# Kernel optimization log

Measured on AMD Instinct MI355X. Metric: run time of the kernel, lower is better.

The kernel has to match this reference:

```python
import jax, jax.numpy as jnp
import numpy as np

B, KD, VD = 65536, 512, 512

def setup_inputs() -> dict:
    key = jax.random.key(0)
    ks = jax.random.split(key, 5)
    return {
        "k": jax.random.normal(ks[0], (B, KD), jnp.float32),
        "v": jax.random.normal(ks[1], (B, VD), jnp.float32),
        "W": jax.random.normal(ks[2], (VD, KD), jnp.float32) * 0.02,  # memory.weight
        "S": jax.random.normal(ks[3], (VD, KD), jnp.float32) * 0.01,  # momentum buffer
        "gate_w": jax.random.normal(ks[4], (3, KD), jnp.float32) * 0.02,
        "gate_b": jnp.full((3,), 0.5, jnp.float32),  # nn.init.constant_(bias, 0.5)
    }

def reference(k, v, W, S, gate_w, gate_b):
    sg = jax.lax.stop_gradient
    # memory lookup: Linear(key_dim -> val_dim), no bias
    retrieved = k @ W.T                           # (B, VD)
    diff = retrieved - sg(v)
    loss_memory = jnp.mean(diff * diff)
    # --- TTT update (training path; all detached from autodiff in torch) ---
    # autograd.grad of mse(memory(k), v) w.r.t. W is analytically an outer product:
    # grad = 2/(B*VD) * (k @ W.T - v).T @ k
    d = sg(diff)                                  # loss_ttt uses detached k, v -> same residual values
    grad = (2.0 / (B * VD)) * (d.T @ sg(k))       # (VD, KD)
    # gates from batch-mean key
    gates = jax.nn.sigmoid(gate_w @ sg(jnp.mean(k, axis=0)) + gate_b)  # (3,)
    alpha, eta, theta = gates[0], gates[1], gates[2]
    new_S = eta * sg(S) - theta * grad            # momentum decay + gradient step
    new_W = (1.0 - alpha) * sg(W) + new_S         # gated weight decay + momentum write
    return retrieved, loss_memory, new_W, new_S
```

## Files before the change

kernel.cpp:

```cpp
#include <hip/hip_runtime.h>
#include <hip/hip_bf16.h>

typedef __attribute__((ext_vector_type(8))) short bf16x8;
typedef __attribute__((ext_vector_type(4))) float f32x4;
typedef unsigned int u32;
typedef unsigned short u16;

#define NB 65536
#define NKD 512
#define NVD 512

#define WS_COLSUM 262144
#define WS_LOSS   262656
#define WS_DIFFT_BYTES 1056768

#define OUT_LOSS 33554432
#define OUT_W    33554433
#define OUT_S    33816577

__device__ inline u32 pkbf2(float a, float b) {
    __hip_bfloat162 h2 = __float22bfloat162_rn(make_float2(a, b));
    u32 r;
    __builtin_memcpy(&r, &h2, 4);
    return r;
}

__device__ inline void async16(const u16* g, u16* l) {
    __builtin_amdgcn_global_load_lds(
        (const __attribute__((address_space(1))) u32*)g,
        (__attribute__((address_space(3))) u32*)l, 16, 0, 0);
}

#define PA 72
#define PT 136

__global__ __launch_bounds__(256, 3)
void k1_gemm1(const float* __restrict__ kmat, const float* __restrict__ vmat,
              const float* __restrict__ Wmat, float* __restrict__ out,
              float* __restrict__ ws, u16* __restrict__ diffT) {
    __shared__ u16 sm[18432];
    __shared__ float lred[4];

    const int tid = threadIdx.x;
    const int bx = blockIdx.x;
    const int xcd = bx & 7, slot = bx >> 3;
    const int rowtile = xcd * 64 + (slot >> 2), ntile = slot & 3;
    const long b0 = (long)rowtile * 128;
    const int vd0 = ntile * 128;
    const int wv = tid >> 6, lane = tid & 63;
    const int wm = wv & 1, wn = wv >> 1;
    const int col = lane & 15, kg = lane >> 4;

    const int srow = tid >> 4;
    const int scol = (tid & 15) * 4;

    f32x4 acc[4][4] = {};

    const float* gA = kmat + (b0 + srow) * 512 + scol;
    const float* gB = Wmat + (long)(vd0 + srow) * 512 + scol;

    float4 ra[8], rb[8];
#pragma unroll
    for (int i = 0; i < 8; ++i) {
        ra[i] = *(const float4*)(gA + (long)i * 16 * 512);
        rb[i] = *(const float4*)(gB + (long)i * 16 * 512);
    }

    for (int it = 0; it < 8; ++it) {
        __syncthreads();
#pragma unroll
        for (int i = 0; i < 8; ++i) {
            int r = i * 16 + srow;
            *(uint2*)&sm[r * PA + scol] = make_uint2(pkbf2(ra[i].x, ra[i].y), pkbf2(ra[i].z, ra[i].w));
            *(uint2*)&sm[9216 + r * PA + scol] = make_uint2(pkbf2(rb[i].x, rb[i].y), pkbf2(rb[i].z, rb[i].w));
        }
        __syncthreads();
        if (it < 7) {
            gA += 64; gB += 64;
#pragma unroll
            for (int i = 0; i < 8; ++i) {
                ra[i] = *(const float4*)(gA + (long)i * 16 * 512);
                rb[i] = *(const float4*)(gB + (long)i * 16 * 512);
            }
        }
#pragma unroll
        for (int kk = 0; kk < 2; ++kk) {
            bf16x8 af[4], bfr[4];
#pragma unroll
            for (int i = 0; i < 4; ++i)
                af[i] = *(const bf16x8*)&sm[(wm * 64 + i * 16 + col) * PA + kk * 32 + kg * 8];
#pragma unroll
            for (int j = 0; j < 4; ++j)
                bfr[j] = *(const bf16x8*)&sm[9216 + (wn * 64 + j * 16 + col) * PA + kk * 32 + kg * 8];
#pragma unroll
            for (int i = 0; i < 4; ++i)
#pragma unroll
                for (int j = 0; j < 4; ++j)
                    acc[i][j] = __builtin_amdgcn_mfma_f32_16x16x32_bf16(af[i], bfr[j], acc[i][j], 0, 0, 0);
        }
    }

    __syncthreads();
    u16* smT = sm;

    float lossp = 0.f;
    const int rg = lane >> 4;
#pragma unroll
    for (int i = 0; i < 4; ++i) {
#pragma unroll
        for (int j = 0; j < 4; ++j) {
            int r0 = wm * 64 + i * 16 + rg * 4;
            int c  = wn * 64 + j * 16 + col;
            long gb = b0 + r0;
            float dd[4];
#pragma unroll
            for (int r = 0; r < 4; ++r) {
                float rv = acc[i][j][r];
                long gidx = (gb + r) * 512 + vd0 + c;
                out[gidx] = rv;
                float dv = rv - vmat[gidx];
                lossp += dv * dv;
                dd[r] = dv;
            }
            *(u32*)&smT[c * PT + r0]     = pkbf2(dd[0], dd[1]);
            *(u32*)&smT[c * PT + r0 + 2] = pkbf2(dd[2], dd[3]);
        }
    }

#pragma unroll
    for (int m = 32; m; m >>= 1) lossp += __shfl_xor(lossp, m);
    if (lane == 0) lred[wv] = lossp;
    __syncthreads();
    if (tid == 0) atomicAdd(&ws[WS_LOSS], lred[0] + lred[1] + lred[2] + lred[3]);

    {
        const int c = tid >> 1, h = tid & 1;
        const u16* src = &smT[c * PT + h * 64];
        u16* dst = diffT + ((long)(vd0 + c) << 16) + b0 + h * 64;
#pragma unroll
        for (int q = 0; q < 8; ++q) {
            uint4 t4 = *(const uint4*)(src + q * 8);
            *(uint4*)(dst + q * 8) = t4;
        }
    }
}

__global__ __launch_bounds__(256, 3)
void k2_grad(const u16* __restrict__ diffT, const float* __restrict__ kmat,
             float* __restrict__ ws) {
    __shared__ u16 sm[25600];

    const int tid = threadIdx.x;
    const int bx = blockIdx.x;
    const int xcd = bx & 7, slot = bx >> 3;
    const int chunk = xcd * 4 + (slot >> 4), tile = slot & 15;
    const int vd0 = (tile >> 2) * 128, kd0 = (tile & 3) * 128;
    const long b0 = (long)chunk * 2048;
    const int wv = tid >> 6, lane = tid & 63;
    const int wm = wv & 1, wn = wv >> 1;
    const int col = lane & 15, kg = lane >> 4;

    const int bcol = (tid & 63) * 2;
    const int bq = wv * 16;

    f32x4 acc[4][4] = {};
    float cs0 = 0.f, cs1 = 0.f;

    const int rowb0 = wv * 32;
    const u16* gAit = diffT + ((long)(vd0 + rowb0 + (lane >> 3)) << 16) + b0 + (lane & 7) * 8;
    const float* gk0 = kmat + (b0 + bq) * 512 + kd0 + bcol;

    float2 rB[16];
#pragma unroll
    for (int q = 0; q < 4; ++q)
        async16(gAit + ((long)(q * 8) << 16), &sm[(rowb0 + q * 8) * 64]);
#pragma unroll
    for (int i = 0; i < 16; ++i) rB[i] = *(const float2*)(gk0 + (long)i * 512);

    for (int it = 0; it < 32; ++it) {
        u16* As = sm + (it & 1) * 8192;
        u16* Bs = sm + 16384;
        __syncthreads();
        {
#pragma unroll
            for (int i = 0; i < 16; ++i) { cs0 += rB[i].x; cs1 += rB[i].y; }
            u32 p0[8], p1[8];
#pragma unroll
            for (int i = 0; i < 8; ++i) {
                p0[i] = pkbf2(rB[2 * i].x, rB[2 * i + 1].x);
                p1[i] = pkbf2(rB[2 * i].y, rB[2 * i + 1].y);
            }
            *(uint4*)&Bs[bcol * PA + bq]           = make_uint4(p0[0], p0[1], p0[2], p0[3]);
            *(uint4*)&Bs[bcol * PA + bq + 8]       = make_uint4(p0[4], p0[5], p0[6], p0[7]);
            *(uint4*)&Bs[(bcol + 1) * PA + bq]     = make_uint4(p1[0], p1[1], p1[2], p1[3]);
            *(uint4*)&Bs[(bcol + 1) * PA + bq + 8] = make_uint4(p1[4], p1[5], p1[6], p1[7]);
        }
        __syncthreads();
        if (it < 31) {
            u16* An = sm + ((it + 1) & 1) * 8192;
            const u16* gan = gAit + (it + 1) * 64;
#pragma unroll
            for (int q = 0; q < 4; ++q)
                async16(gan + ((long)(q * 8) << 16), &An[(rowb0 + q * 8) * 64]);
            const float* gkn = gk0 + (long)(it + 1) * 64 * 512;
#pragma unroll
            for (int i = 0; i < 16; ++i) rB[i] = *(const float2*)(gkn + (long)i * 512);
        }
#pragma unroll
        for (int kk = 0; kk < 2; ++kk) {
            bf16x8 af[4], bfr[4];
#pragma unroll
            for (int i = 0; i < 4; ++i)
                af[i] = *(const bf16x8*)&As[(wm * 64 + i * 16 + col) * 64 + kk * 32 + kg * 8];
#pragma unroll
            for (int j = 0; j < 4; ++j)
                bfr[j] = *(const bf16x8*)&Bs[(wn * 64 + j * 16 + col) * PA + kk * 32 + kg * 8];
#pragma unroll
            for (int i = 0; i < 4; ++i)
#pragma unroll
                for (int j = 0; j < 4; ++j)
                    acc[i][j] = __builtin_amdgcn_mfma_f32_16x16x32_bf16(af[i], bfr[j], acc[i][j], 0, 0, 0);
        }
    }

    const int rg = lane >> 4;
#pragma unroll
    for (int i = 0; i < 4; ++i)
#pragma unroll
        for (int j = 0; j < 4; ++j)
#pragma unroll
            for (int r = 0; r < 4; ++r) {
                int vd = vd0 + wm * 64 + i * 16 + rg * 4 + r;
                int kd = kd0 + wn * 64 + j * 16 + col;
                atomicAdd(&ws[vd * 512 + kd], acc[i][j][r]);
            }

    if (vd0 == 0) {
        __syncthreads();
        float* cred = (float*)sm;
        cred[bcol * 4 + wv] = cs0;
        cred[(bcol + 1) * 4 + wv] = cs1;
        __syncthreads();
        if (tid < 128) {
            float s = cred[tid * 4] + cred[tid * 4 + 1] + cred[tid * 4 + 2] + cred[tid * 4 + 3];
            atomicAdd(&ws[WS_COLSUM + kd0 + tid], s);
        }
    }
}

__global__ __launch_bounds__(256)
void k3_final(const float* __restrict__ Wmat, const float* __restrict__ Smat,
              const float* __restrict__ gw, const float* __restrict__ gb,
              const float* __restrict__ ws, float* __restrict__ out) {
    __shared__ float gates[3];
    const int tid = threadIdx.x;
    if (tid < 64) {
        float d0 = 0.f, d1 = 0.f, d2 = 0.f;
#pragma unroll
        for (int i = 0; i < 8; ++i) {
            int kd = i * 64 + tid;
            float km = ws[WS_COLSUM + kd] * (1.0f / 65536.0f);
            d0 += gw[kd] * km;
            d1 += gw[512 + kd] * km;
            d2 += gw[1024 + kd] * km;
        }
#pragma unroll
        for (int m = 32; m; m >>= 1) {
            d0 += __shfl_xor(d0, m);
            d1 += __shfl_xor(d1, m);
            d2 += __shfl_xor(d2, m);
        }
        if (tid == 0) {
            gates[0] = 1.f / (1.f + __expf(-(d0 + gb[0])));
            gates[1] = 1.f / (1.f + __expf(-(d1 + gb[1])));
            gates[2] = 1.f / (1.f + __expf(-(d2 + gb[2])));
        }
    }
    __syncthreads();
    const float alpha = gates[0], eta = gates[1], theta = gates[2];
    const int i = blockIdx.x * 256 + tid;
    float g = ws[i] * 5.9604644775390625e-8f;
    float ns = eta * Smat[i] - theta * g;
    out[OUT_S + i] = ns;
    out[OUT_W + i] = (1.f - alpha) * Wmat[i] + ns;
    if (blockIdx.x == 0 && tid == 0)
        out[OUT_LOSS] = ws[WS_LOSS] * 2.98023223876953125e-8f;
}

extern "C" void kernel_launch(void* const* d_in, const int* in_sizes, int n_in,
                              void* d_out, int out_size, void* d_ws, size_t ws_size,
                              hipStream_t stream) {
    const float* k  = (const float*)d_in[0];
    const float* v  = (const float*)d_in[1];
    const float* W  = (const float*)d_in[2];
    const float* S  = (const float*)d_in[3];
    const float* gw = (const float*)d_in[4];
    const float* gb = (const float*)d_in[5];
    float* out = (float*)d_out;
    float* ws  = (float*)d_ws;
    u16* diffT = (u16*)((char*)d_ws + WS_DIFFT_BYTES);

    hipMemsetAsync(d_ws, 0, (WS_LOSS + 1) * sizeof(float), stream);

    hipLaunchKernelGGL(k1_gemm1, dim3(2048), dim3(256), 0, stream, k, v, W, out, ws, diffT);
    hipLaunchKernelGGL(k2_grad,  dim3(512),  dim3(256), 0, stream, diffT, k, ws);
    hipLaunchKernelGGL(k3_final, dim3(1024), dim3(256), 0, stream, W, S, gw, gb, ws, out);
}
```

Before: 490.6 us.

## Compute gradient via k^T k and v^T k Gram matrices, fusing both GEMM passes

Rewrites the gradient algebraically as W·(kᵀk) − vᵀk. Both Gram matrices are computed straight from the inputs in the same launch as the retrieval GEMM, so the bf16 transposed diff buffer and its round trip through memory are gone. The final kernel now does a 512x512x512 matmul (W times kᵀk) on CUDA cores before the elementwise update. In exchange the reduction work doubles, since two Gram matrices replace one diffᵀk, and the final kernel becomes compute heavy. Accuracy also changes because the residual is no longer formed explicitly before bf16 rounding.

```diff
diff --git a/kernel.cpp b/kernel.cpp
--- a/kernel.cpp
+++ b/kernel.cpp
@@ -6,17 +6,17 @@
 typedef unsigned int u32;
 typedef unsigned short u16;
 
-#define NB 65536
-#define NKD 512
-#define NVD 512
-
+#define WS_G2     0
 #define WS_COLSUM 262144
 #define WS_LOSS   262656
-#define WS_DIFFT_BYTES 1056768
+#define WS_G1     262912
+#define WS_END    525056
 
 #define OUT_LOSS 33554432
 #define OUT_W    33554433
 #define OUT_S    33816577
+
+#define PA 72
 
 __device__ inline u32 pkbf2(float a, float b) {
     __hip_bfloat162 h2 = __float22bfloat162_rn(make_float2(a, b));
@@ -25,225 +25,200 @@
     return r;
 }
 
-__device__ inline void async16(const u16* g, u16* l) {
-    __builtin_amdgcn_global_load_lds(
-        (const __attribute__((address_space(1))) u32*)g,
-        (__attribute__((address_space(3))) u32*)l, 16, 0, 0);
-}
-
-#define PA 72
-#define PT 136
-
 __global__ __launch_bounds__(256, 3)
-void k1_gemm1(const float* __restrict__ kmat, const float* __restrict__ vmat,
-              const float* __restrict__ Wmat, float* __restrict__ out,
-              float* __restrict__ ws, u16* __restrict__ diffT) {
+void k12(const float* __restrict__ kmat, const float* __restrict__ vmat,
+         const float* __restrict__ Wmat, float* __restrict__ out,
+         float* __restrict__ ws) {
     __shared__ u16 sm[18432];
-    __shared__ float lred[4];
+    __shared__ float red[4];
 
     const int tid = threadIdx.x;
     const int bx = blockIdx.x;
-    const int xcd = bx & 7, slot = bx >> 3;
-    const int rowtile = xcd * 64 + (slot >> 2), ntile = slot & 3;
-    const long b0 = (long)rowtile * 128;
-    const int vd0 = ntile * 128;
+    const int g24 = bx / 24;
+    const int u   = bx - g24 * 24;
     const int wv = tid >> 6, lane = tid & 63;
     const int wm = wv & 1, wn = wv >> 1;
     const int col = lane & 15, kg = lane >> 4;
-
-    const int srow = tid >> 4;
-    const int scol = (tid & 15) * 4;
-
-    f32x4 acc[4][4] = {};
-
-    const float* gA = kmat + (b0 + srow) * 512 + scol;
-    const float* gB = Wmat + (long)(vd0 + srow) * 512 + scol;
-
-    float4 ra[8], rb[8];
-#pragma unroll
-    for (int i = 0; i < 8; ++i) {
-        ra[i] = *(const float4*)(gA + (long)i * 16 * 512);
-        rb[i] = *(const float4*)(gB + (long)i * 16 * 512);
-    }
-
-    for (int it = 0; it < 8; ++it) {
+    const int rg = lane >> 4;
+
+    if (u < 16) {
+        const int idx = g24 * 16 + u;
+        const int xcd = idx & 7, slot = idx >> 3;
+        const int rowtile = xcd * 64 + (slot >> 2), ntile = slot & 3;
+        const long b0 = (long)rowtile * 128;
+        const int vd0 = ntile * 128;
+
+        const int srow = tid >> 4;
+        const int scol = (tid & 15) * 4;
+
+        f32x4 acc[4][4] = {};
+
+        const float* gA = kmat + (b0 + srow) * 512 + scol;
+        const float* gB = Wmat + (long)(vd0 + srow) * 512 + scol;
+
+        float4 ra[8], rb[8];
+#pragma unroll
+        for (int i = 0; i < 8; ++i) {
+            ra[i] = *(const float4*)(gA + (long)i * 16 * 512);
+            rb[i] = *(const float4*)(gB + (long)i * 16 * 512);
+        }
+
+        for (int it = 0; it < 8; ++it) {
+            __syncthreads();
+#pragma unroll
+            for (int i = 0; i < 8; ++i) {
+                int r = i * 16 + srow;
+                *(uint2*)&sm[r * PA + scol] = make_uint2(pkbf2(ra[i].x, ra[i].y), pkbf2(ra[i].z, ra[i].w));
+                *(uint2*)&sm[9216 + r * PA + scol] = make_uint2(pkbf2(rb[i].x, rb[i].y), pkbf2(rb[i].z, rb[i].w));
+            }
+            __syncthreads();
+            if (it < 7) {
+                gA += 64; gB += 64;
+#pragma unroll
+                for (int i = 0; i < 8; ++i) {
+                    ra[i] = *(const float4*)(gA + (long)i * 16 * 512);
+                    rb[i] = *(const float4*)(gB + (long)i * 16 * 512);
+                }
+            }
+#pragma unroll
+            for (int kk = 0; kk < 2; ++kk) {
+                bf16x8 af[4], bfr[4];
+#pragma unroll
+                for (int i = 0; i < 4; ++i)
+                    af[i] = *(const bf16x8*)&sm[(wm * 64 + i * 16 + col) * PA + kk * 32 + kg * 8];
+#pragma unroll
+                for (int j = 0; j < 4; ++j)
+                    bfr[j] = *(const bf16x8*)&sm[9216 + (wn * 64 + j * 16 + col) * PA + kk * 32 + kg * 8];
+#pragma unroll
+                for (int i = 0; i < 4; ++i)
+#pragma unroll
+                    for (int j = 0; j < 4; ++j)
+                        acc[i][j] = __builtin_amdgcn_mfma_f32_16x16x32_bf16(af[i], bfr[j], acc[i][j], 0, 0, 0);
+            }
+        }
+
+        float lossp = 0.f;
+#pragma unroll
+        for (int i = 0; i < 4; ++i) {
+#pragma unroll
+            for (int j = 0; j < 4; ++j) {
+                int r0 = wm * 64 + i * 16 + rg * 4;
+                int c  = wn * 64 + j * 16 + col;
+                long gb = b0 + r0;
+#pragma unroll
+                for (int r = 0; r < 4; ++r) {
+                    float rv = acc[i][j][r];
+                    long gidx = (gb + r) * 512 + vd0 + c;
+                    out[gidx] = rv;
+                    float dv = rv - vmat[gidx];
+                    lossp += dv * dv;
+                }
+            }
+        }
+#pragma unroll
+        for (int m = 32; m; m >>= 1) lossp += __shfl_xor(lossp, m);
+        if (lane == 0) red[wv] = lossp;
         __syncthreads();
-#pragma unroll
-        for (int i = 0; i < 8; ++i) {
-            int r = i * 16 + srow;
-            *(uint2*)&sm[r * PA + scol] = make_uint2(pkbf2(ra[i].x, ra[i].y), pkbf2(ra[i].z, ra[i].w));
-            *(uint2*)&sm[9216 + r * PA + scol] = make_uint2(pkbf2(rb[i].x, rb[i].y), pkbf2(rb[i].z, rb[i].w));
-        }
-        __syncthreads();
-        if (it < 7) {
-            gA += 64; gB += 64;
-#pragma unroll
-            for (int i = 0; i < 8; ++i) {
-                ra[i] = *(const float4*)(gA + (long)i * 16 * 512);
-                rb[i] = *(const float4*)(gB + (long)i * 16 * 512);
-            }
-        }
-#pragma unroll
-        for (int kk = 0; kk < 2; ++kk) {
-            bf16x8 af[4], bfr[4];
-#pragma unroll
-            for (int i = 0; i < 4; ++i)
-                af[i] = *(const bf16x8*)&sm[(wm * 64 + i * 16 + col) * PA + kk * 32 + kg * 8];
+        if (tid == 0) atomicAdd(&ws[WS_LOSS], red[0] + red[1] + red[2] + red[3]);
+
+    } else {
+        const int idx = g24 * 8 + (u - 16);
+        const int xcd = idx & 7, slot = idx >> 3;
+        const int chunk = xcd * 4 + (slot >> 5);
+        const int ot = slot & 31;
+        const int pi = ot >> 4;
+        const int i0 = ((ot >> 2) & 3) * 128;
+        const int j0 = (ot & 3) * 128;
+        const long b0 = (long)chunk * 2048;
+
+        const float* Asrc = pi ? vmat : kmat;
+        const int bcol = (tid & 63) * 2;
+        const int bq = wv * 16;
+
+        f32x4 acc[4][4] = {};
+        float cs0 = 0.f, cs1 = 0.f;
+
+        const float* gA0 = Asrc + (b0 + bq) * 512 + i0 + bcol;
+        const float* gB0 = kmat + (b0 + bq) * 512 + j0 + bcol;
+
+        float2 rA[16], rB[16];
+#pragma unroll
+        for (int i = 0; i < 16; ++i) {
+            rA[i] = *(const float2*)(gA0 + (long)i * 512);
+            rB[i] = *(const float2*)(gB0 + (long)i * 512);
+        }
+
+        for (int it = 0; it < 32; ++it) {
+            __syncthreads();
+            {
+                u32 a0[8], a1[8], p0[8], p1[8];
+#pragma unroll
+                for (int i = 0; i < 16; ++i) { cs0 += rB[i].x; cs1 += rB[i].y; }
+#pragma unroll
+                for (int i = 0; i < 8; ++i) {
+                    a0[i] = pkbf2(rA[2 * i].x, rA[2 * i + 1].x);
+                    a1[i] = pkbf2(rA[2 * i].y, rA[2 * i + 1].y);
+                    p0[i] = pkbf2(rB[2 * i].x, rB[2 * i + 1].x);
+                    p1[i] = pkbf2(rB[2 * i].y, rB[2 * i + 1].y);
+                }
+                *(uint4*)&sm[bcol * PA + bq]           = make_uint4(a0[0], a0[1], a0[2], a0[3]);
+                *(uint4*)&sm[bcol * PA + bq + 8]       = make_uint4(a0[4], a0[5], a0[6], a0[7]);
+                *(uint4*)&sm[(bcol + 1) * PA + bq]     = make_uint4(a1[0], a1[1], a1[2], a1[3]);
+                *(uint4*)&sm[(bcol + 1) * PA + bq + 8] = make_uint4(a1[4], a1[5], a1[6], a1[7]);
+                *(uint4*)&sm[9216 + bcol * PA + bq]           = make_uint4(p0[0], p0[1], p0[2], p0[3]);
+                *(uint4*)&sm[9216 + bcol * PA + bq + 8]       = make_uint4(p0[4], p0[5], p0[6], p0[7]);
+                *(uint4*)&sm[9216 + (bcol + 1) * PA + bq]     = make_uint4(p1[0], p1[1], p1[2], p1[3]);
+                *(uint4*)&sm[9216 + (bcol + 1) * PA + bq + 8] = make_uint4(p1[4], p1[5], p1[6], p1[7]);
+            }
+            __syncthreads();
+            if (it < 31) {
+                const float* gan = gA0 + (long)(it + 1) * 64 * 512;
+                const float* gbn = gB0 + (long)(it + 1) * 64 * 512;
+#pragma unroll
+                for (int i = 0; i < 16; ++i) {
+                    rA[i] = *(const float2*)(gan + (long)i * 512);
+                    rB[i] = *(const float2*)(gbn + (long)i * 512);
+                }
+            }
+#pragma unroll
+            for (int kk = 0; kk < 2; ++kk) {
+                bf16x8 af[4], bfr[4];
+#pragma unroll
+                for (int i = 0; i < 4; ++i)
+                    af[i] = *(const bf16x8*)&sm[(wm * 64 + i * 16 + col) * PA + kk * 32 + kg * 8];
+#pragma unroll
+                for (int j = 0; j < 4; ++j)
+                    bfr[j] = *(const bf16x8*)&sm[9216 + (wn * 64 + j * 16 + col) * PA + kk * 32 + kg * 8];
+#pragma unroll
+                for (int i = 0; i < 4; ++i)
+#pragma unroll
+                    for (int j = 0; j < 4; ++j)
+                        acc[i][j] = __builtin_amdgcn_mfma_f32_16x16x32_bf16(af[i], bfr[j], acc[i][j], 0, 0, 0);
+            }
+        }
+
+        float* G = ws + (pi ? WS_G2 : WS_G1);
+#pragma unroll
+        for (int i = 0; i < 4; ++i)
 #pragma unroll
             for (int j = 0; j < 4; ++j)
-                bfr[j] = *(const bf16x8*)&sm[9216 + (wn * 64 + j * 16 + col) * PA + kk * 32 + kg * 8];
-#pragma unroll
-            for (int i = 0; i < 4; ++i)
-#pragma unroll
-                for (int j = 0; j < 4; ++j)
-                    acc[i][j] = __builtin_amdgcn_mfma_f32_16x16x32_bf16(af[i], bfr[j], acc[i][j], 0, 0, 0);
-        }
-    }
-
-    __syncthreads();
-    u16* smT = sm;
-
-    float lossp = 0.f;
-    const int rg = lane >> 4;
-#pragma unroll
-    for (int i = 0; i < 4; ++i) {
-#pragma unroll
-        for (int j = 0; j < 4; ++j) {
-            int r0 = wm * 64 + i * 16 + rg * 4;
-            int c  = wn * 64 + j * 16 + col;
-            long gb = b0 + r0;
-            float dd[4];
-#pragma unroll
-            for (int r = 0; r < 4; ++r) {
-                float rv = acc[i][j][r];
-                long gidx = (gb + r) * 512 + vd0 + c;
-                out[gidx] = rv;
-                float dv = rv - vmat[gidx];
-                lossp += dv * dv;
-                dd[r] = dv;
-            }
-            *(u32*)&smT[c * PT + r0]     = pkbf2(dd[0], dd[1]);
-            *(u32*)&smT[c * PT + r0 + 2] = pkbf2(dd[2], dd[3]);
-        }
-    }
-
-#pragma unroll
-    for (int m = 32; m; m >>= 1) lossp += __shfl_xor(lossp, m);
-    if (lane == 0) lred[wv] = lossp;
-    __syncthreads();
-    if (tid == 0) atomicAdd(&ws[WS_LOSS], lred[0] + lred[1] + lred[2] + lred[3]);
-
-    {
-        const int c = tid >> 1, h = tid & 1;
-        const u16* src = &smT[c * PT + h * 64];
-        u16* dst = diffT + ((long)(vd0 + c) << 16) + b0 + h * 64;
-#pragma unroll
-        for (int q = 0; q < 8; ++q) {
-            uint4 t4 = *(const uint4*)(src + q * 8);
-            *(uint4*)(dst + q * 8) = t4;
-        }
-    }
-}
-
-__global__ __launch_bounds__(256, 3)
-void k2_grad(const u16* __restrict__ diffT, const float* __restrict__ kmat,
-             float* __restrict__ ws) {
-    __shared__ u16 sm[25600];
-
-    const int tid = threadIdx.x;
-    const int bx = blockIdx.x;
-    const int xcd = bx & 7, slot = bx >> 3;
-    const int chunk = xcd * 4 + (slot >> 4), tile = slot & 15;
-    const int vd0 = (tile >> 2) * 128, kd0 = (tile & 3) * 128;
-    const long b0 = (long)chunk * 2048;
-    const int wv = tid >> 6, lane = tid & 63;
-    const int wm = wv & 1, wn = wv >> 1;
-    const int col = lane & 15, kg = lane >> 4;
-
-    const int bcol = (tid & 63) * 2;
-    const int bq = wv * 16;
-
-    f32x4 acc[4][4] = {};
-    float cs0 = 0.f, cs1 = 0.f;
-
-    const int rowb0 = wv * 32;
-    const u16* gAit = diffT + ((long)(vd0 + rowb0 + (lane >> 3)) << 16) + b0 + (lane & 7) * 8;
-    const float* gk0 = kmat + (b0 + bq) * 512 + kd0 + bcol;
-
-    float2 rB[16];
-#pragma unroll
-    for (int q = 0; q < 4; ++q)
-        async16(gAit + ((long)(q * 8) << 16), &sm[(rowb0 + q * 8) * 64]);
-#pragma unroll
-    for (int i = 0; i < 16; ++i) rB[i] = *(const float2*)(gk0 + (long)i * 512);
-
-    for (int it = 0; it < 32; ++it) {
-        u16* As = sm + (it & 1) * 8192;
-        u16* Bs = sm + 16384;
-        __syncthreads();
-        {
-#pragma unroll
-            for (int i = 0; i < 16; ++i) { cs0 += rB[i].x; cs1 += rB[i].y; }
-            u32 p0[8], p1[8];
-#pragma unroll
-            for (int i = 0; i < 8; ++i) {
-                p0[i] = pkbf2(rB[2 * i].x, rB[2 * i + 1].x);
-                p1[i] = pkbf2(rB[2 * i].y, rB[2 * i + 1].y);
-            }
-            *(uint4*)&Bs[bcol * PA + bq]           = make_uint4(p0[0], p0[1], p0[2], p0[3]);
-            *(uint4*)&Bs[bcol * PA + bq + 8]       = make_uint4(p0[4], p0[5], p0[6], p0[7]);
-            *(uint4*)&Bs[(bcol + 1) * PA + bq]     = make_uint4(p1[0], p1[1], p1[2], p1[3]);
-            *(uint4*)&Bs[(bcol + 1) * PA + bq + 8] = make_uint4(p1[4], p1[5], p1[6], p1[7]);
-        }
-        __syncthreads();
-        if (it < 31) {
-            u16* An = sm + ((it + 1) & 1) * 8192;
-            const u16* gan = gAit + (it + 1) * 64;
-#pragma unroll
-            for (int q = 0; q < 4; ++q)
-                async16(gan + ((long)(q * 8) << 16), &An[(rowb0 + q * 8) * 64]);
-            const float* gkn = gk0 + (long)(it + 1) * 64 * 512;
-#pragma unroll
-            for (int i = 0; i < 16; ++i) rB[i] = *(const float2*)(gkn + (long)i * 512);
-        }
-#pragma unroll
-        for (int kk = 0; kk < 2; ++kk) {
-            bf16x8 af[4], bfr[4];
-#pragma unroll
-            for (int i = 0; i < 4; ++i)
-                af[i] = *(const bf16x8*)&As[(wm * 64 + i * 16 + col) * 64 + kk * 32 + kg * 8];
-#pragma unroll
-            for (int j = 0; j < 4; ++j)
-                bfr[j] = *(const bf16x8*)&Bs[(wn * 64 + j * 16 + col) * PA + kk * 32 + kg * 8];
-#pragma unroll
-            for (int i = 0; i < 4; ++i)
-#pragma unroll
-                for (int j = 0; j < 4; ++j)
-                    acc[i][j] = __builtin_amdgcn_mfma_f32_16x16x32_bf16(af[i], bfr[j], acc[i][j], 0, 0, 0);
-        }
-    }
-
-    const int rg = lane >> 4;
-#pragma unroll
-    for (int i = 0; i < 4; ++i)
-#pragma unroll
-        for (int j = 0; j < 4; ++j)
-#pragma unroll
-            for (int r = 0; r < 4; ++r) {
-                int vd = vd0 + wm * 64 + i * 16 + rg * 4 + r;
-                int kd = kd0 + wn * 64 + j * 16 + col;
-                atomicAdd(&ws[vd * 512 + kd], acc[i][j][r]);
-            }
-
-    if (vd0 == 0) {
-        __syncthreads();
-        float* cred = (float*)sm;
-        cred[bcol * 4 + wv] = cs0;
-        cred[(bcol + 1) * 4 + wv] = cs1;
-        __syncthreads();
-        if (tid < 128) {
-            float s = cred[tid * 4] + cred[tid * 4 + 1] + cred[tid * 4 + 2] + cred[tid * 4 + 3];
-            atomicAdd(&ws[WS_COLSUM + kd0 + tid], s);
+#pragma unroll
+                for (int r = 0; r < 4; ++r) {
+                    int orow = i0 + wm * 64 + i * 16 + rg * 4 + r;
+                    int ocol = j0 + wn * 64 + j * 16 + col;
+                    atomicAdd(&G[orow * 512 + ocol], acc[i][j][r]);
+                }
+
+        if (ot < 4) {
+            __syncthreads();
+            float* cred = (float*)sm;
+            cred[bcol * 4 + wv] = cs0;
+            cred[(bcol + 1) * 4 + wv] = cs1;
+            __syncthreads();
+            if (tid < 128) {
+                float s = cred[tid * 4] + cred[tid * 4 + 1] + cred[tid * 4 + 2] + cred[tid * 4 + 3];
+                atomicAdd(&ws[WS_COLSUM + j0 + tid], s);
+            }
         }
     }
 }
@@ -253,7 +228,13 @@
               const float* __restrict__ gw, const float* __restrict__ gb,
               const float* __restrict__ ws, float* __restrict__ out) {
     __shared__ float gates[3];
+    __shared__ float wrow[512];
     const int tid = threadIdx.x;
+    const int vd = blockIdx.x;
+
+    wrow[tid]       = Wmat[vd * 512 + tid];
+    wrow[tid + 256] = Wmat[vd * 512 + tid + 256];
+
     if (tid < 64) {
         float d0 = 0.f, d1 = 0.f, d2 = 0.f;
 #pragma unroll
@@ -278,12 +259,30 @@
     }
     __syncthreads();
     const float alpha = gates[0], eta = gates[1], theta = gates[2];
-    const int i = blockIdx.x * 256 + tid;
-    float g = ws[i] * 5.9604644775390625e-8f;
-    float ns = eta * Smat[i] - theta * g;
-    out[OUT_S + i] = ns;
-    out[OUT_W + i] = (1.f - alpha) * Wmat[i] + ns;
-    if (blockIdx.x == 0 && tid == 0)
+
+    const float* G1 = ws + WS_G1;
+    float g0 = 0.f, g1 = 0.f;
+#pragma unroll 4
+    for (int c = 0; c < 512; ++c) {
+        float wc = wrow[c];
+        g0 += wc * G1[c * 512 + tid];
+        g1 += wc * G1[c * 512 + tid + 256];
+    }
+    {
+        int i = vd * 512 + tid;
+        float g = (g0 - ws[WS_G2 + i]) * 5.9604644775390625e-8f;
+        float ns = eta * Smat[i] - theta * g;
+        out[OUT_S + i] = ns;
+        out[OUT_W + i] = (1.f - alpha) * wrow[tid] + ns;
+    }
+    {
+        int i = vd * 512 + tid + 256;
+        float g = (g1 - ws[WS_G2 + i]) * 5.9604644775390625e-8f;
+        float ns = eta * Smat[i] - theta * g;
+        out[OUT_S + i] = ns;
+        out[OUT_W + i] = (1.f - alpha) * wrow[tid + 256] + ns;
+    }
+    if (vd == 0 && tid == 0)
         out[OUT_LOSS] = ws[WS_LOSS] * 2.98023223876953125e-8f;
 }
 
@@ -298,11 +297,9 @@
     const float* gb = (const float*)d_in[5];
     float* out = (float*)d_out;
     float* ws  = (float*)d_ws;
-    u16* diffT = (u16*)((char*)d_ws + WS_DIFFT_BYTES);
-
-    hipMemsetAsync(d_ws, 0, (WS_LOSS + 1) * sizeof(float), stream);
-
-    hipLaunchKernelGGL(k1_gemm1, dim3(2048), dim3(256), 0, stream, k, v, W, out, ws, diffT);
-    hipLaunchKernelGGL(k2_grad,  dim3(512),  dim3(256), 0, stream, diffT, k, ws);
-    hipLaunchKernelGGL(k3_final, dim3(1024), dim3(256), 0, stream, W, S, gw, gb, ws, out);
+
+    hipMemsetAsync(d_ws, 0, WS_END * sizeof(float), stream);
+
+    hipLaunchKernelGGL(k12,      dim3(3072), dim3(256), 0, stream, k, v, W, out, ws);
+    hipLaunchKernelGGL(k3_final, dim3(512),  dim3(256), 0, stream, W, S, gw, gb, ws, out);
 }
```

New measurement: 665.9 us. +35.7%, slower.
